# Performance work log

Measured on AMD Instinct MI355X. Metric: run time of the kernel, lower is better.

The kernel has to match this reference:

```python
import jax, jax.numpy as jnp
import numpy as np

D = 1024      # embed_dim
E = 2048      # expand * embed_dim
S_DIM = 128   # shrunken attn dim s
C = 256       # chunk size
SRC = 4096    # src_len
G = SRC // C  # num chunks
B = 8
STD = 0.02


def setup_inputs() -> dict:
    key = jax.random.key(0)
    ks = jax.random.split(key, 16)
    n = lambda k, shp: jax.random.normal(k, shp, dtype=jnp.float32)
    inp = {
        "query": n(ks[0], (SRC, B, D)),
        "key":   n(ks[1], (SRC, B, D)),
        "value": n(ks[2], (SRC, B, D)),
        # learned params (torch Linear stored as [in, out])
        "Wxs": n(ks[3], (D, S_DIM)) * STD, "bxs": n(ks[4], (S_DIM,)) * STD,
        "Wve": n(ks[5], (D, E)) * STD,     "bve": n(ks[6], (E,)) * STD,
        "Wue": n(ks[7], (D, E)) * STD,     "bue": n(ks[8], (E,)) * STD,
        "Wod": n(ks[9], (E, D)) * STD,     "bod": n(ks[10], (D,)) * STD,
        "rel_bias": n(ks[11], (C,)) * STD,
        "gamma": n(ks[12], (4, S_DIM)) * STD,
        "beta":  n(ks[13], (4, S_DIM)) * STD,
    }
    return inp


def reference(query, key, value, Wxs, bxs, Wve, bve, Wue, bue, Wod, bod,
              rel_bias, gamma, beta):
    # [S, B, D] -> [B, G, C, D]
    x = jnp.transpose(value, (1, 0, 2)).reshape(B, G, C, D)
    v = jnp.tanh(x @ Wve + bve)          # [b,g,c,e]
    z = jnp.tanh(x @ Wxs + bxs)          # [b,g,c,s]
    q_quad = z * gamma[0] + beta[0]
    k_quad = z * gamma[1] + beta[1]
    q_lin  = z * gamma[2] + beta[2]
    k_lin  = z * gamma[3] + beta[3]
    # local quadratic attention: relu(qk + bias)^2
    qk = jnp.einsum('bgns,bgms->bgnm', q_quad, k_quad)
    a = jnp.square(jax.nn.relu(qk + rel_bias))
    v_quad = jnp.einsum('bgnm,bgme->bgne', a, v)
    # global linear attention
    kv = jnp.einsum('bgcs,bgce->bse', k_lin, v)
    v_lin = jnp.einsum('bgcs,bse->bgce', q_lin, kv)
    u = jnp.tanh(x @ Wue + bue)          # [b,g,c,e]
    o = (u * (v_quad + v_lin)) @ Wod + bod   # [b,g,c,d]
    o = o.reshape(B, G * C, D)
    return jnp.transpose(o, (1, 0, 2))   # [S, B, D]
```

## Files before the change

### kernel.cpp

```cpp
#include <hip/hip_runtime.h>
#include <hip/hip_bf16.h>

using u16 = unsigned short;
using u32 = unsigned int;

typedef __attribute__((ext_vector_type(8))) short bf8;
typedef __attribute__((ext_vector_type(4))) float f4;
typedef __attribute__((ext_vector_type(4))) u16  us4;

#define DEV static __device__ __forceinline__

DEV float bf2f(u16 u) { return __uint_as_float(((u32)u) << 16); }
DEV u16 f2bf(float f) {
    u32 x = __float_as_uint(f);
    x += 0x7FFFu + ((x >> 16) & 1u);
    return (u16)(x >> 16);
}
DEV float tanhf_fast(float x) {
    float e = __expf(2.0f * x);
    return 1.0f - 2.0f / (e + 1.0f);
}
DEV f4 MFMA(bf8 a, bf8 b, f4 c) {
    return __builtin_amdgcn_mfma_f32_16x16x32_bf16(a, b, c, 0, 0, 0);
}
DEV int xcd_swz(int bx, int nwg) { return (bx & 7) * (nwg >> 3) + (bx >> 3); }

DEV void gload16(const u16* src, u16* dst) {
    __builtin_amdgcn_global_load_lds(
        (const __attribute__((address_space(1))) void*)src,
        (__attribute__((address_space(3))) void*)dst, 16, 0, 0);
}

#define SBAR()  __builtin_amdgcn_s_barrier()
#define SCHED() __builtin_amdgcn_sched_barrier(0)


#define WS_XB    ((size_t)0)
#define WS_WXST  ((size_t)67108864)
#define WS_WVET  ((size_t)67371008)
#define WS_WUET  ((size_t)71565312)
#define WS_WODT  ((size_t)75759616)
#define WS_KVT   ((size_t)79953920)
#define WS_A     ((size_t)84148224)
#define WS_QL    ((size_t)100925440)
#define WS_VT    ((size_t)109314048)
#define WS_T1    ((size_t)243531776)
#define WS_Z     ((size_t)243531776)
#define WS_KLT   ((size_t)251920384)
#define WS_QQ    ((size_t)260308992)
#define WS_KQ    ((size_t)268697600)
#define WS_KVF   ((size_t)277086208)

DEV void stage128x64(const u16* __restrict__ gbase, int ld, u16* lds, int w, int lane) {
    const int srow = lane >> 3;
    const int scol = ((lane & 7) ^ srow) * 8;
    #pragma unroll
    for (int i = 0; i < 4; i++) {
        const int rt = (i * 4 + w) * 8 + srow;
        gload16(gbase + (size_t)rt * ld + scol, lds + (size_t)(i * 4 + w) * 512);
    }
}

DEV void frag_mfma_64_swz(const u16* As, const u16* Bs, int wm, int wn, int ln, int lh,
                          f4 acc[4][4]) {
    #pragma unroll
    for (int kk2 = 0; kk2 < 2; kk2++) {
        const int sx = (((kk2 << 2) + lh) ^ (ln & 7)) << 3;
        bf8 a[4], b[4];
        #pragma unroll
        for (int mt = 0; mt < 4; mt++)
            a[mt] = *reinterpret_cast<const bf8*>(As + (wm * 64 + mt * 16 + ln) * 64 + sx);
        #pragma unroll
        for (int nt = 0; nt < 4; nt++)
            b[nt] = *reinterpret_cast<const bf8*>(Bs + (wn * 64 + nt * 16 + ln) * 64 + sx);
        #pragma unroll
        for (int mt = 0; mt < 4; mt++)
            #pragma unroll
            for (int nt = 0; nt < 4; nt++)
                acc[mt][nt] = MFMA(a[mt], b[nt], acc[mt][nt]);
    }
}

template<int NT, typename FA, typename FB>
DEV void gemm_pipe(FA stageA, FB stageB, u16* As, u16* Bs,
                   int wm, int wn, int ln, int lh, f4 acc[4][4]) {
    stageA(As, 0); stageB(Bs, 0);
    #pragma unroll 2
    for (int t = 0; t + 1 < NT; ++t) {
        u16* An = As + ((t & 1) ^ 1) * 8192;
        u16* Bn = Bs + ((t & 1) ^ 1) * 8192;
        stageA(An, t + 1); stageB(Bn, t + 1);
        asm volatile("s_waitcnt vmcnt(8)" ::: "memory");
        SBAR(); SCHED();
        frag_mfma_64_swz(As + (t & 1) * 8192, Bs + (t & 1) * 8192, wm, wn, ln, lh, acc);
        SCHED(); SBAR(); SCHED();
    }
    asm volatile("s_waitcnt vmcnt(0)" ::: "memory");
    SBAR();
    frag_mfma_64_swz(As + ((NT - 1) & 1) * 8192, Bs + ((NT - 1) & 1) * 8192, wm, wn, ln, lh, acc);
    SBAR();
}


#define T256 16384

DEV void stage2(const u16* __restrict__ gbase, int ld, u16* lds, int tid, int i0, int i1) {
    const int slot = tid & 7;
    {
        const int row = i0 * 64 + (tid >> 3);
        gload16(gbase + (size_t)row * ld + ((slot ^ (row & 7)) << 3),
                lds + ((size_t)(i0 * 512 + (tid & ~63)) << 3));
    }
    {
        const int row = i1 * 64 + (tid >> 3);
        gload16(gbase + (size_t)row * ld + ((slot ^ (row & 7)) << 3),
                lds + ((size_t)(i1 * 512 + (tid & ~63)) << 3));
    }
}

DEV const bf8* frag_ptr(const u16* base, int row, int ks, int lh) {
    const int slot = ((ks << 2) + lh) ^ (row & 7);
    return reinterpret_cast<const bf8*>(base + row * 64 + slot * 8);
}

template<int NT, typename FA, typename FB>
DEV void gemm_pipe8(FA sA, FB sB, u16* As, u16* Bs,
                    int wm, int wn, int ln, int lh, f4 acc[8][4]) {
    sA(As, 0, 0, 2); sA(As, 0, 1, 3); sB(Bs, 0, 0, 1); sB(Bs, 0, 2, 3);
    if (NT > 1) {
        sA(As + T256, 1, 0, 2); sA(As + T256, 1, 1, 3);
        sB(Bs + T256, 1, 0, 1); sB(Bs + T256, 1, 2, 3);
        asm volatile("s_waitcnt vmcnt(8)" ::: "memory");
    } else {
        asm volatile("s_waitcnt vmcnt(0)" ::: "memory");
    }
    SBAR(); SCHED();
    #pragma unroll 2
    for (int t = 0; t < NT; ++t) {
        const int c = t & 1;
        const u16* Ab = As + c * T256;
        const u16* Bb = Bs + c * T256;
        u16* Ac = As + c * T256;
        u16* Bc = Bs + c * T256;
        bf8 aR[8], b0[4], b1[4];
        #pragma unroll
        for (int j = 0; j < 4; j++) {
            aR[j]     = *frag_ptr(Ab, wm * 128 + j * 16 + ln, 0, lh);
            aR[4 + j] = *frag_ptr(Ab, wm * 128 + j * 16 + ln, 1, lh);
        }
        #pragma unroll
        for (int k = 0; k < 2; k++) {
            b0[k]     = *frag_ptr(Bb, wn * 64 + k * 16 + ln, 0, lh);
            b0[2 + k] = *frag_ptr(Bb, wn * 64 + k * 16 + ln, 1, lh);
        }
        SBAR(); SCHED();
        __builtin_amdgcn_s_setprio(1);
        #pragma unroll
        for (int j = 0; j < 4; j++) { acc[j][0] = MFMA(aR[j], b0[0], acc[j][0]);
                                      acc[j][1] = MFMA(aR[j], b0[1], acc[j][1]); }
        #pragma unroll
        for (int j = 0; j < 4; j++) { acc[j][0] = MFMA(aR[4 + j], b0[2], acc[j][0]);
                                      acc[j][1] = MFMA(aR[4 + j], b0[3], acc[j][1]); }
        __builtin_amdgcn_s_setprio(0);
        SCHED();
        #pragma unroll
        for (int k = 0; k < 2; k++) {
            b1[k]     = *frag_ptr(Bb, wn * 64 + (2 + k) * 16 + ln, 0, lh);
            b1[2 + k] = *frag_ptr(Bb, wn * 64 + (2 + k) * 16 + ln, 1, lh);
        }
        SBAR(); SCHED();
        __builtin_amdgcn_s_setprio(1);
        #pragma unroll
        for (int j = 0; j < 4; j++) { acc[j][2] = MFMA(aR[j], b1[0], acc[j][2]);
                                      acc[j][3] = MFMA(aR[j], b1[1], acc[j][3]); }
        #pragma unroll
        for (int j = 0; j < 4; j++) { acc[j][2] = MFMA(aR[4 + j], b1[2], acc[j][2]);
                                      acc[j][3] = MFMA(aR[4 + j], b1[3], acc[j][3]); }
        __builtin_amdgcn_s_setprio(0);
        SCHED();
        #pragma unroll
        for (int j = 0; j < 4; j++) {
            aR[j]     = *frag_ptr(Ab, wm * 128 + 64 + j * 16 + ln, 0, lh);
            aR[4 + j] = *frag_ptr(Ab, wm * 128 + 64 + j * 16 + ln, 1, lh);
        }
        if (t + 2 < NT) { sA(Ac, t + 2, 0, 2); sB(Bc, t + 2, 0, 1); }
        SBAR(); SCHED();
        __builtin_amdgcn_s_setprio(1);
        #pragma unroll
        for (int j = 0; j < 4; j++) { acc[4 + j][0] = MFMA(aR[j], b0[0], acc[4 + j][0]);
                                      acc[4 + j][1] = MFMA(aR[j], b0[1], acc[4 + j][1]); }
        #pragma unroll
        for (int j = 0; j < 4; j++) { acc[4 + j][0] = MFMA(aR[4 + j], b0[2], acc[4 + j][0]);
                                      acc[4 + j][1] = MFMA(aR[4 + j], b0[3], acc[4 + j][1]); }
        __builtin_amdgcn_s_setprio(0);
        SCHED();
        if (t + 2 < NT) {
            sA(Ac, t + 2, 1, 3); sB(Bc, t + 2, 2, 3);
            asm volatile("s_waitcnt vmcnt(8)" ::: "memory");
        } else if (t + 1 < NT) {
            asm volatile("s_waitcnt vmcnt(0)" ::: "memory");
        }
        SBAR(); SCHED();
        __builtin_amdgcn_s_setprio(1);
        #pragma unroll
        for (int j = 0; j < 4; j++) { acc[4 + j][2] = MFMA(aR[j], b1[0], acc[4 + j][2]);
                                      acc[4 + j][3] = MFMA(aR[j], b1[1], acc[4 + j][3]); }
        #pragma unroll
        for (int j = 0; j < 4; j++) { acc[4 + j][2] = MFMA(aR[4 + j], b1[2], acc[4 + j][2]);
                                      acc[4 + j][3] = MFMA(aR[4 + j], b1[3], acc[4 + j][3]); }
        __builtin_amdgcn_s_setprio(0);
        SCHED();
    }
}

__global__ void k_cvt_x(const float* __restrict__ src, u16* __restrict__ dst) {
    int m = blockIdx.x;
    int s = m >> 3, b = m & 7;
    const float* in = src + (size_t)m * 1024;
    u16* outp = dst + (((size_t)b << 12) + s) * 1024;
    int t = threadIdx.x * 4;
    float4 v = *reinterpret_cast<const float4*>(in + t);
    us4 o; o[0] = f2bf(v.x); o[1] = f2bf(v.y); o[2] = f2bf(v.z); o[3] = f2bf(v.w);
    *reinterpret_cast<us4*>(outp + t) = o;
}

__global__ void k_transpose(const float* __restrict__ src, u16* __restrict__ dst, int R, int C) {
    __shared__ u16 tile[32][33];
    int tx = threadIdx.x & 31, ty = threadIdx.x >> 5;
    int r0 = blockIdx.y * 32, c0 = blockIdx.x * 32;
    #pragma unroll
    for (int rr = ty; rr < 32; rr += 8)
        tile[rr][tx] = f2bf(src[(size_t)(r0 + rr) * C + c0 + tx]);
    __syncthreads();
    #pragma unroll
    for (int cc = ty; cc < 32; cc += 8)
        dst[(size_t)(c0 + cc) * R + r0 + tx] = tile[tx][cc];
}

__global__ void k_klinT(const u16* __restrict__ z, const float* __restrict__ gamma,
                        const float* __restrict__ beta, u16* __restrict__ klt) {
    __shared__ u16 tile[32][33];
    int tx = threadIdx.x & 31, ty = threadIdx.x >> 5;
    int r0 = blockIdx.x * 32;
    int c0 = blockIdx.y * 32;
    float gs = gamma[384 + c0 + tx], bs = beta[384 + c0 + tx];
    #pragma unroll
    for (int rr = ty; rr < 32; rr += 8) {
        u16 zv = z[(size_t)(r0 + rr) * 128 + c0 + tx];
        tile[rr][tx] = f2bf(bf2f(zv) * gs + bs);
    }
    __syncthreads();
    int b = r0 >> 12;
    int pos0 = r0 & 4095;
    #pragma unroll
    for (int cc = ty; cc < 32; cc += 8)
        klt[(((size_t)b * 128 + c0 + cc) << 12) + pos0 + tx] = tile[tx][cc];
}

__global__ __launch_bounds__(256) void k_zgemm(const u16* __restrict__ xb, const u16* __restrict__ WxsT,
                                               const float* __restrict__ bxs,
                                               const float* __restrict__ gamma, const float* __restrict__ beta,
                                               u16* __restrict__ z, u16* __restrict__ qq,
                                               u16* __restrict__ kq, u16* __restrict__ ql) {
    __shared__ u16 As[2][128 * 64];
    __shared__ u16 Bs[2][128 * 64];
    const int tid = threadIdx.x;
    const int lane = tid & 63, w = tid >> 6;
    const int ln = lane & 15, lh = lane >> 4;
    const int wm = w >> 1, wn = w & 1;
    const int rowbase = xcd_swz(blockIdx.x, 256) * 128;
    const u16* Ab = xb + (size_t)rowbase * 1024;
    f4 acc[4][4] = {};
    gemm_pipe<16>(
        [&](u16* l, int t) { stage128x64(Ab + t * 64, 1024, l, w, lane); },
        [&](u16* l, int t) { stage128x64(WxsT + t * 64, 1024, l, w, lane); },
        As[0], Bs[0], wm, wn, ln, lh, acc);
    #pragma unroll
    for (int mt = 0; mt < 4; mt++)
        #pragma unroll
        for (int nt = 0; nt < 4; nt++) {
            int col = wn * 64 + nt * 16 + ln;
            float bias = bxs[col];
            float g0 = gamma[col],       b0 = beta[col];
            float g1 = gamma[128 + col], b1 = beta[128 + col];
            float g2 = gamma[256 + col], b2 = beta[256 + col];
            int r0 = rowbase + wm * 64 + mt * 16 + lh * 4;
            #pragma unroll
            for (int rg = 0; rg < 4; rg++) {
                float zv = tanhf_fast(acc[mt][nt][rg] + bias);
                size_t idx = ((size_t)(r0 + rg) << 7) + col;
                z[idx]  = f2bf(zv);
                qq[idx] = f2bf(zv * g0 + b0);
                kq[idx] = f2bf(zv * g1 + b1);
                ql[idx] = f2bf(zv * g2 + b2);
            }
        }
}

__global__ __launch_bounds__(512, 2) void k_vgemm(const u16* __restrict__ xb, const u16* __restrict__ WveT,
                                                  const float* __restrict__ bve, u16* __restrict__ vT) {
    __shared__ u16 As[2 * T256];
    __shared__ u16 Bs[2 * T256];
    const int tid = threadIdx.x;
    const int lane = tid & 63, w = tid >> 6;
    const int ln = lane & 15, lh = lane >> 4;
    const int wm = w >> 2, wn = w & 3;
    const int rowbase = xcd_swz(blockIdx.x, 128) * 256;
    const int colbase = blockIdx.y * 256;
    const u16* Ag = xb + (size_t)rowbase * 1024;
    const u16* Bg = WveT + (size_t)colbase * 1024;
    f4 acc[8][4] = {};
    gemm_pipe8<16>(
        [&](u16* l, int t, int i0, int i1) { stage2(Ag + t * 64, 1024, l, tid, i0, i1); },
        [&](u16* l, int t, int i0, int i1) { stage2(Bg + t * 64, 1024, l, tid, i0, i1); },
        As, Bs, wm, wn, ln, lh, acc);
    #pragma unroll
    for (int mt = 0; mt < 8; mt++)
        #pragma unroll
        for (int nt = 0; nt < 4; nt++) {
            int e = colbase + wn * 64 + nt * 16 + ln;
            float bias = bve[e];
            int r0 = rowbase + wm * 128 + mt * 16 + lh * 4;
            int bb = r0 >> 12, s0 = r0 & 4095;
            us4 p;
            #pragma unroll
            for (int rg = 0; rg < 4; rg++) p[rg] = f2bf(tanhf_fast(acc[mt][nt][rg] + bias));
            *reinterpret_cast<us4*>(vT + (((size_t)bb * 2048 + e) << 12) + s0) = p;
        }
}

__global__ __launch_bounds__(256) void k_kv(const u16* __restrict__ vT, const u16* __restrict__ klt,
                                            float* __restrict__ kvF) {
    __shared__ u16 As[2][128 * 64];
    __shared__ u16 Bs[2][128 * 64];
    const int tid = threadIdx.x;
    const int lane = tid & 63, w = tid >> 6;
    const int ln = lane & 15, lh = lane >> 4;
    const int wm = w >> 1, wn = w & 1;
    const int b = blockIdx.z;
    const int rowbase = blockIdx.x * 128;
    const int kbase = blockIdx.y * 1024;
    const u16* Ab = vT + ((size_t)b * 2048 + rowbase) * 4096 + kbase;
    const u16* Bb = klt + ((size_t)b * 128) * 4096 + kbase;
    f4 acc[4][4] = {};
    gemm_pipe<16>(
        [&](u16* l, int t) { stage128x64(Ab + t * 64, 4096, l, w, lane); },
        [&](u16* l, int t) { stage128x64(Bb + t * 64, 4096, l, w, lane); },
        As[0], Bs[0], wm, wn, ln, lh, acc);
    #pragma unroll
    for (int mt = 0; mt < 4; mt++)
        #pragma unroll
        for (int nt = 0; nt < 4; nt++) {
            int s = wn * 64 + nt * 16 + ln;
            int e0 = rowbase + wm * 64 + mt * 16 + lh * 4;
            #pragma unroll
            for (int rg = 0; rg < 4; rg++)
                atomicAdd(&kvF[(((size_t)b * 2048 + e0 + rg) << 7) + s], acc[mt][nt][rg]);
        }
}

__global__ void k_kvcvt(const float* __restrict__ kvF, u16* __restrict__ kvT, int n) {
    int i = (blockIdx.x * blockDim.x + threadIdx.x) * 4;
    if (i < n) {
        float4 v = *reinterpret_cast<const float4*>(kvF + i);
        us4 o; o[0] = f2bf(v.x); o[1] = f2bf(v.y); o[2] = f2bf(v.z); o[3] = f2bf(v.w);
        *reinterpret_cast<us4*>(kvT + i) = o;
    }
}

__global__ __launch_bounds__(256) void k_a(const u16* __restrict__ qq, const u16* __restrict__ kq,
                                           const float* __restrict__ rel_bias, u16* __restrict__ a_out) {
    const int lane = threadIdx.x & 63, wid = threadIdx.x >> 6;
    const int ln = lane & 15, lh = lane >> 4;
    const int wm = wid >> 1, wn = wid & 1;
    const int ci = blockIdx.y;
    const int qbase = blockIdx.x * 128 + wm * 64;
    const int nbase = wn * 128;
    const int rowbase = ci << 8;
    f4 acc[4][8] = {};
    const u16* qr[4];
    #pragma unroll
    for (int mt = 0; mt < 4; mt++) qr[mt] = qq + ((size_t)(rowbase + qbase + mt * 16 + ln) << 7);
    const u16* kr[8];
    #pragma unroll
    for (int nt = 0; nt < 8; nt++) kr[nt] = kq + ((size_t)(rowbase + nbase + nt * 16 + ln) << 7);
    #pragma unroll
    for (int kk = 0; kk < 128; kk += 32) {
        int k0 = kk + lh * 8;
        bf8 aq[4], ak[8];
        #pragma unroll
        for (int mt = 0; mt < 4; mt++) aq[mt] = *reinterpret_cast<const bf8*>(qr[mt] + k0);
        #pragma unroll
        for (int nt = 0; nt < 8; nt++) ak[nt] = *reinterpret_cast<const bf8*>(kr[nt] + k0);
        #pragma unroll
        for (int mt = 0; mt < 4; mt++)
            #pragma unroll
            for (int nt = 0; nt < 8; nt++)
                acc[mt][nt] = MFMA(aq[mt], ak[nt], acc[mt][nt]);
    }
    #pragma unroll
    for (int nt = 0; nt < 8; nt++) {
        int key = nbase + nt * 16 + ln;
        float rb = rel_bias[key];
        #pragma unroll
        for (int mt = 0; mt < 4; mt++) {
            int r0 = qbase + mt * 16 + lh * 4;
            #pragma unroll
            for (int rg = 0; rg < 4; rg++) {
                float v = acc[mt][nt][rg] + rb;
                v = fmaxf(v, 0.0f); v = v * v;
                a_out[((size_t)ci << 16) + ((size_t)(r0 + rg) << 8) + key] = f2bf(v);
            }
        }
    }
}

__global__ __launch_bounds__(512, 2) void k_t1(const u16* __restrict__ ql, const u16* __restrict__ a_in,
                                               const u16* __restrict__ vT, const u16* __restrict__ kvT,
                                               u16* __restrict__ t1) {
    __shared__ u16 As[2 * T256];
    __shared__ u16 Bs[2 * T256];
    const int tid = threadIdx.x;
    const int lane = tid & 63, w = tid >> 6;
    const int ln = lane & 15, lh = lane >> 4;
    const int wm = w >> 2, wn = w & 3;
    const int ci = xcd_swz(blockIdx.x, 128);
    const int rowbase = ci << 8;
    const int ebase = blockIdx.y * 256;
    const int b = ci >> 4, g = ci & 15;
    const u16* Aa = ql + (size_t)rowbase * 128;
    const u16* Ba = kvT + ((size_t)(b * 2048 + ebase)) * 128;
    const u16* Ab2 = a_in + ((size_t)ci << 16);
    const u16* Bb2 = vT + ((size_t)(b * 2048 + ebase)) * 4096 + (g << 8);
    f4 acc[8][4] = {};
    gemm_pipe8<6>(
        [&](u16* l, int t, int i0, int i1) {
            if (t < 2) stage2(Aa + t * 64, 128, l, tid, i0, i1);
            else       stage2(Ab2 + (t - 2) * 64, 256, l, tid, i0, i1);
        },
        [&](u16* l, int t, int i0, int i1) {
            if (t < 2) stage2(Ba + t * 64, 128, l, tid, i0, i1);
            else       stage2(Bb2 + (t - 2) * 64, 4096, l, tid, i0, i1);
        },
        As, Bs, wm, wn, ln, lh, acc);
    #pragma unroll
    for (int mt = 0; mt < 8; mt++)
        #pragma unroll
        for (int nt = 0; nt < 4; nt++) {
            int e = ebase + wn * 64 + nt * 16 + ln;
            int r0 = rowbase + wm * 128 + mt * 16 + lh * 4;
            #pragma unroll
            for (int rg = 0; rg < 4; rg++)
                t1[((size_t)(r0 + rg) << 11) + e] = f2bf(acc[mt][nt][rg]);
        }
}

__global__ __launch_bounds__(512, 2) void k_u(const u16* __restrict__ xb, const u16* __restrict__ WueT,
                                              const float* __restrict__ bue, u16* t1) {
    __shared__ u16 As[2 * T256];
    __shared__ u16 Bs[2 * T256];
    const int tid = threadIdx.x;
    const int lane = tid & 63, w = tid >> 6;
    const int ln = lane & 15, lh = lane >> 4;
    const int wm = w >> 2, wn = w & 3;
    const int rowbase = xcd_swz(blockIdx.x, 128) * 256;
    const int colbase = blockIdx.y * 256;
    const u16* Ag = xb + (size_t)rowbase * 1024;
    const u16* Bg = WueT + (size_t)colbase * 1024;
    f4 acc[8][4] = {};
    gemm_pipe8<16>(
        [&](u16* l, int t, int i0, int i1) { stage2(Ag + t * 64, 1024, l, tid, i0, i1); },
        [&](u16* l, int t, int i0, int i1) { stage2(Bg + t * 64, 1024, l, tid, i0, i1); },
        As, Bs, wm, wn, ln, lh, acc);
    #pragma unroll
    for (int mt = 0; mt < 8; mt++)
        #pragma unroll
        for (int nt = 0; nt < 4; nt++) {
            int e = colbase + wn * 64 + nt * 16 + ln;
            float bias = bue[e];
            int r0 = rowbase + wm * 128 + mt * 16 + lh * 4;
            #pragma unroll
            for (int rg = 0; rg < 4; rg++) {
                size_t idx = ((size_t)(r0 + rg) << 11) + e;
                float t = bf2f(t1[idx]);
                float u = tanhf_fast(acc[mt][nt][rg] + bias);
                t1[idx] = f2bf(u * t);
            }
        }
}

__global__ __launch_bounds__(512, 2) void k_o(const u16* __restrict__ t1, const u16* __restrict__ WodT,
                                              const float* __restrict__ bod, float* __restrict__ out) {
    __shared__ u16 As[2 * T256];
    __shared__ u16 Bs[2 * T256];
    const int tid = threadIdx.x;
    const int lane = tid & 63, w = tid >> 6;
    const int ln = lane & 15, lh = lane >> 4;
    const int wm = w >> 2, wn = w & 3;
    const int rowbase = xcd_swz(blockIdx.x, 128) * 256;
    const int colbase = blockIdx.y * 256;
    const u16* Ag = t1 + (size_t)rowbase * 2048;
    const u16* Bg = WodT + (size_t)colbase * 2048;
    f4 acc[8][4] = {};
    gemm_pipe8<32>(
        [&](u16* l, int t, int i0, int i1) { stage2(Ag + t * 64, 2048, l, tid, i0, i1); },
        [&](u16* l, int t, int i0, int i1) { stage2(Bg + t * 64, 2048, l, tid, i0, i1); },
        As, Bs, wm, wn, ln, lh, acc);
    #pragma unroll
    for (int mt = 0; mt < 8; mt++)
        #pragma unroll
        for (int nt = 0; nt < 4; nt++) {
            int d = colbase + wn * 64 + nt * 16 + ln;
            float bias = bod[d];
            int r0 = rowbase + wm * 128 + mt * 16 + lh * 4;
            #pragma unroll
            for (int rg = 0; rg < 4; rg++) {
                int r = r0 + rg;
                int s = r & 4095, bb = r >> 12;
                out[((size_t)(s * 8 + bb) << 10) + d] = acc[mt][nt][rg] + bias;
            }
        }
}

extern "C" void kernel_launch(void* const* d_in, const int* in_sizes, int n_in,
                              void* d_out, int out_size, void* d_ws, size_t ws_size,
                              hipStream_t stream) {
    const float* value = (const float*)d_in[2];
    const float* Wxs = (const float*)d_in[3];  const float* bxs = (const float*)d_in[4];
    const float* Wve = (const float*)d_in[5];  const float* bve = (const float*)d_in[6];
    const float* Wue = (const float*)d_in[7];  const float* bue = (const float*)d_in[8];
    const float* Wod = (const float*)d_in[9];  const float* bod = (const float*)d_in[10];
    const float* rel_bias = (const float*)d_in[11];
    const float* gamma = (const float*)d_in[12];
    const float* beta  = (const float*)d_in[13];
    float* out = (float*)d_out;

    char* ws = (char*)d_ws;
    u16* xb   = (u16*)(ws + WS_XB);
    u16* WxsT = (u16*)(ws + WS_WXST);
    u16* WveT = (u16*)(ws + WS_WVET);
    u16* WueT = (u16*)(ws + WS_WUET);
    u16* WodT = (u16*)(ws + WS_WODT);
    u16* kvT  = (u16*)(ws + WS_KVT);
    u16* a    = (u16*)(ws + WS_A);
    u16* ql   = (u16*)(ws + WS_QL);
    u16* vT   = (u16*)(ws + WS_VT);
    u16* t1   = (u16*)(ws + WS_T1);
    u16* z    = (u16*)(ws + WS_Z);
    u16* klt  = (u16*)(ws + WS_KLT);
    u16* qq   = (u16*)(ws + WS_QQ);
    u16* kq   = (u16*)(ws + WS_KQ);
    float* kvF = (float*)(ws + WS_KVF);

    k_cvt_x<<<32768, 256, 0, stream>>>(value, xb);
    k_transpose<<<dim3(4, 32),  256, 0, stream>>>(Wxs, WxsT, 1024, 128);
    k_transpose<<<dim3(64, 32), 256, 0, stream>>>(Wve, WveT, 1024, 2048);
    k_transpose<<<dim3(64, 32), 256, 0, stream>>>(Wue, WueT, 1024, 2048);
    k_transpose<<<dim3(32, 64), 256, 0, stream>>>(Wod, WodT, 2048, 1024);
    k_zgemm<<<256, 256, 0, stream>>>(xb, WxsT, bxs, gamma, beta, z, qq, kq, ql);
    k_klinT<<<dim3(1024, 4), 256, 0, stream>>>(z, gamma, beta, klt);
    k_vgemm<<<dim3(128, 8), 512, 0, stream>>>(xb, WveT, bve, vT);
    hipMemsetAsync(kvF, 0, (size_t)8 * 2048 * 128 * 4, stream);
    k_kv<<<dim3(16, 4, 8), 256, 0, stream>>>(vT, klt, kvF);
    k_kvcvt<<<2048, 256, 0, stream>>>(kvF, kvT, 8 * 2048 * 128);
    k_a<<<dim3(2, 128), 256, 0, stream>>>(qq, kq, rel_bias, a);
    k_t1<<<dim3(128, 8), 512, 0, stream>>>(ql, a, vT, kvT, t1);
    k_u<<<dim3(128, 8), 512, 0, stream>>>(xb, WueT, bue, t1);
    k_o<<<dim3(128, 4), 512, 0, stream>>>(t1, WodT, bod, out);
}
```

Baseline: 750.6 us.

## Make big GEMMs persistent with 256 blocks looping over column tiles

The v, u and output projection GEMMs now launch 256 workgroups (one per CU on the device) instead of 1024 or 512. Each workgroup keeps its row tile and walks several 256-wide column tiles inside one continuous software pipeline. A per-tile epilogue writes results and resets the accumulators between tiles. The aim is to remove tail effects and the pipeline prologue and epilogue drains at tile boundaries, and to reuse the A rows from cache. The cost is that epilogue stores now sit inside the pipelined loop and may stall it, and the old XCD swizzle is replaced by a new block mapping.

```diff
diff --git a/kernel.cpp b/kernel.cpp
--- a/kernel.cpp
+++ b/kernel.cpp
@@ -24,6 +24,10 @@
     return __builtin_amdgcn_mfma_f32_16x16x32_bf16(a, b, c, 0, 0, 0);
 }
 DEV int xcd_swz(int bx, int nwg) { return (bx & 7) * (nwg >> 3) + (bx >> 3); }
+DEV void persist_map(int bx, int& row, int& grp) {
+    row = ((bx >> 3) << 2) | ((bx >> 1) & 3);
+    grp = bx & 1;
+}
 
 DEV void gload16(const u16* src, u16* dst) {
     __builtin_amdgcn_global_load_lds(
@@ -123,9 +127,10 @@
     return reinterpret_cast<const bf8*>(base + row * 64 + slot * 8);
 }
 
-template<int NT, typename FA, typename FB>
-DEV void gemm_pipe8(FA sA, FB sB, u16* As, u16* Bs,
+template<int NT, int PSHIFT, typename FA, typename FB, typename FE>
+DEV void gemm_pipe8(FA sA, FB sB, FE epi, u16* As, u16* Bs,
                     int wm, int wn, int ln, int lh, f4 acc[8][4]) {
+    constexpr int PMASK = (1 << PSHIFT) - 1;
     sA(As, 0, 0, 2); sA(As, 0, 1, 3); sB(Bs, 0, 0, 1); sB(Bs, 0, 2, 3);
     if (NT > 1) {
         sA(As + T256, 1, 0, 2); sA(As + T256, 1, 1, 3);
@@ -135,9 +140,7 @@
         asm volatile("s_waitcnt vmcnt(0)" ::: "memory");
     }
     SBAR(); SCHED();
-    #pragma unroll 2
-    for (int t = 0; t < NT; ++t) {
-        const int c = t & 1;
+    auto body = [&](int t, const int c) {
         const u16* Ab = As + c * T256;
         const u16* Bb = Bs + c * T256;
         u16* Ac = As + c * T256;
@@ -210,6 +213,12 @@
                                       acc[4 + j][3] = MFMA(aR[4 + j], b1[3], acc[4 + j][3]); }
         __builtin_amdgcn_s_setprio(0);
         SCHED();
+    };
+    for (int t = 0; t < NT; t += 2) {
+        body(t, 0);
+        if ((t & PMASK) == PMASK) epi(t >> PSHIFT);
+        body(t + 1, 1);
+        if (((t + 1) & PMASK) == PMASK) epi((t + 1) >> PSHIFT);
     }
 }
 
@@ -305,28 +314,37 @@
     const int lane = tid & 63, w = tid >> 6;
     const int ln = lane & 15, lh = lane >> 4;
     const int wm = w >> 2, wn = w & 3;
-    const int rowbase = xcd_swz(blockIdx.x, 128) * 256;
-    const int colbase = blockIdx.y * 256;
+    int rowt, grp;
+    persist_map(blockIdx.x, rowt, grp);
+    const int rowbase = rowt * 256;
+    const int grpcol = grp * 1024;
     const u16* Ag = xb + (size_t)rowbase * 1024;
-    const u16* Bg = WveT + (size_t)colbase * 1024;
+    const u16* Bg = WveT + (size_t)grpcol * 1024;
     f4 acc[8][4] = {};
-    gemm_pipe8<16>(
-        [&](u16* l, int t, int i0, int i1) { stage2(Ag + t * 64, 1024, l, tid, i0, i1); },
-        [&](u16* l, int t, int i0, int i1) { stage2(Bg + t * 64, 1024, l, tid, i0, i1); },
+    gemm_pipe8<64, 4>(
+        [&](u16* l, int T, int i0, int i1) { stage2(Ag + (T & 15) * 64, 1024, l, tid, i0, i1); },
+        [&](u16* l, int T, int i0, int i1) {
+            stage2(Bg + (((size_t)(T >> 4)) << 18) + (T & 15) * 64, 1024, l, tid, i0, i1); },
+        [&](int p) {
+            const int colbase = grpcol + p * 256;
+            #pragma unroll
+            for (int mt = 0; mt < 8; mt++)
+                #pragma unroll
+                for (int nt = 0; nt < 4; nt++) {
+                    int e = colbase + wn * 64 + nt * 16 + ln;
+                    float bias = bve[e];
+                    int r0 = rowbase + wm * 128 + mt * 16 + lh * 4;
+                    int bb = r0 >> 12, s0 = r0 & 4095;
+                    us4 pk;
+                    #pragma unroll
+                    for (int rg = 0; rg < 4; rg++) {
+                        pk[rg] = f2bf(tanhf_fast(acc[mt][nt][rg] + bias));
+                        acc[mt][nt][rg] = 0.0f;
+                    }
+                    *reinterpret_cast<us4*>(vT + (((size_t)bb * 2048 + e) << 12) + s0) = pk;
+                }
+        },
         As, Bs, wm, wn, ln, lh, acc);
-    #pragma unroll
-    for (int mt = 0; mt < 8; mt++)
-        #pragma unroll
-        for (int nt = 0; nt < 4; nt++) {
-            int e = colbase + wn * 64 + nt * 16 + ln;
-            float bias = bve[e];
-            int r0 = rowbase + wm * 128 + mt * 16 + lh * 4;
-            int bb = r0 >> 12, s0 = r0 & 4095;
-            us4 p;
-            #pragma unroll
-            for (int rg = 0; rg < 4; rg++) p[rg] = f2bf(tanhf_fast(acc[mt][nt][rg] + bias));
-            *reinterpret_cast<us4*>(vT + (((size_t)bb * 2048 + e) << 12) + s0) = p;
-        }
 }
 
 __global__ __launch_bounds__(256) void k_kv(const u16* __restrict__ vT, const u16* __restrict__ klt,
@@ -433,7 +451,7 @@
     const u16* Ab2 = a_in + ((size_t)ci << 16);
     const u16* Bb2 = vT + ((size_t)(b * 2048 + ebase)) * 4096 + (g << 8);
     f4 acc[8][4] = {};
-    gemm_pipe8<6>(
+    gemm_pipe8<6, 10>(
         [&](u16* l, int t, int i0, int i1) {
             if (t < 2) stage2(Aa + t * 64, 128, l, tid, i0, i1);
             else       stage2(Ab2 + (t - 2) * 64, 256, l, tid, i0, i1);
@@ -442,6 +460,7 @@
             if (t < 2) stage2(Ba + t * 64, 128, l, tid, i0, i1);
             else       stage2(Bb2 + (t - 2) * 64, 4096, l, tid, i0, i1);
         },
+        [&](int) {},
         As, Bs, wm, wn, ln, lh, acc);
     #pragma unroll
     for (int mt = 0; mt < 8; mt++)
@@ -463,30 +482,37 @@
     const int lane = tid & 63, w = tid >> 6;
     const int ln = lane & 15, lh = lane >> 4;
     const int wm = w >> 2, wn = w & 3;
-    const int rowbase = xcd_swz(blockIdx.x, 128) * 256;
-    const int colbase = blockIdx.y * 256;
+    int rowt, grp;
+    persist_map(blockIdx.x, rowt, grp);
+    const int rowbase = rowt * 256;
+    const int grpcol = grp * 1024;
     const u16* Ag = xb + (size_t)rowbase * 1024;
-    const u16* Bg = WueT + (size_t)colbase * 1024;
+    const u16* Bg = WueT + (size_t)grpcol * 1024;
     f4 acc[8][4] = {};
-    gemm_pipe8<16>(
-        [&](u16* l, int t, int i0, int i1) { stage2(Ag + t * 64, 1024, l, tid, i0, i1); },
-        [&](u16* l, int t, int i0, int i1) { stage2(Bg + t * 64, 1024, l, tid, i0, i1); },
+    gemm_pipe8<64, 4>(
+        [&](u16* l, int T, int i0, int i1) { stage2(Ag + (T & 15) * 64, 1024, l, tid, i0, i1); },
+        [&](u16* l, int T, int i0, int i1) {
+            stage2(Bg + (((size_t)(T >> 4)) << 18) + (T & 15) * 64, 1024, l, tid, i0, i1); },
+        [&](int p) {
+            const int colbase = grpcol + p * 256;
+            #pragma unroll
+            for (int mt = 0; mt < 8; mt++)
+                #pragma unroll
+                for (int nt = 0; nt < 4; nt++) {
+                    int e = colbase + wn * 64 + nt * 16 + ln;
+                    float bias = bue[e];
+                    int r0 = rowbase + wm * 128 + mt * 16 + lh * 4;
+                    #pragma unroll
+                    for (int rg = 0; rg < 4; rg++) {
+                        size_t idx = ((size_t)(r0 + rg) << 11) + e;
+                        float t = bf2f(t1[idx]);
+                        float u = tanhf_fast(acc[mt][nt][rg] + bias);
+                        t1[idx] = f2bf(u * t);
+                        acc[mt][nt][rg] = 0.0f;
+                    }
+                }
+        },
         As, Bs, wm, wn, ln, lh, acc);
-    #pragma unroll
-    for (int mt = 0; mt < 8; mt++)
-        #pragma unroll
-        for (int nt = 0; nt < 4; nt++) {
-            int e = colbase + wn * 64 + nt * 16 + ln;
-            float bias = bue[e];
-            int r0 = rowbase + wm * 128 + mt * 16 + lh * 4;
-            #pragma unroll
-            for (int rg = 0; rg < 4; rg++) {
-                size_t idx = ((size_t)(r0 + rg) << 11) + e;
-                float t = bf2f(t1[idx]);
-                float u = tanhf_fast(acc[mt][nt][rg] + bias);
-                t1[idx] = f2bf(u * t);
-            }
-        }
 }
 
 __global__ __launch_bounds__(512, 2) void k_o(const u16* __restrict__ t1, const u16* __restrict__ WodT,
@@ -497,29 +523,36 @@
     const int lane = tid & 63, w = tid >> 6;
     const int ln = lane & 15, lh = lane >> 4;
     const int wm = w >> 2, wn = w & 3;
-    const int rowbase = xcd_swz(blockIdx.x, 128) * 256;
-    const int colbase = blockIdx.y * 256;
+    int rowt, grp;
+    persist_map(blockIdx.x, rowt, grp);
+    const int rowbase = rowt * 256;
+    const int grpcol = grp * 512;
     const u16* Ag = t1 + (size_t)rowbase * 2048;
-    const u16* Bg = WodT + (size_t)colbase * 2048;
+    const u16* Bg = WodT + (size_t)grpcol * 2048;
     f4 acc[8][4] = {};
-    gemm_pipe8<32>(
-        [&](u16* l, int t, int i0, int i1) { stage2(Ag + t * 64, 2048, l, tid, i0, i1); },
-        [&](u16* l, int t, int i0, int i1) { stage2(Bg + t * 64, 2048, l, tid, i0, i1); },
+    gemm_pipe8<64, 5>(
+        [&](u16* l, int T, int i0, int i1) { stage2(Ag + (T & 31) * 64, 2048, l, tid, i0, i1); },
+        [&](u16* l, int T, int i0, int i1) {
+            stage2(Bg + (size_t)(T >> 5) * 524288 + (T & 31) * 64, 2048, l, tid, i0, i1); },
+        [&](int p) {
+            const int colbase = grpcol + p * 256;
+            #pragma unroll
+            for (int mt = 0; mt < 8; mt++)
+                #pragma unroll
+                for (int nt = 0; nt < 4; nt++) {
+                    int d = colbase + wn * 64 + nt * 16 + ln;
+                    float bias = bod[d];
+                    int r0 = rowbase + wm * 128 + mt * 16 + lh * 4;
+                    #pragma unroll
+                    for (int rg = 0; rg < 4; rg++) {
+                        int r = r0 + rg;
+                        int s = r & 4095, bb = r >> 12;
+                        out[((size_t)(s * 8 + bb) << 10) + d] = acc[mt][nt][rg] + bias;
+                        acc[mt][nt][rg] = 0.0f;
+                    }
+                }
+        },
         As, Bs, wm, wn, ln, lh, acc);
-    #pragma unroll
-    for (int mt = 0; mt < 8; mt++)
-        #pragma unroll
-        for (int nt = 0; nt < 4; nt++) {
-            int d = colbase + wn * 64 + nt * 16 + ln;
-            float bias = bod[d];
-            int r0 = rowbase + wm * 128 + mt * 16 + lh * 4;
-            #pragma unroll
-            for (int rg = 0; rg < 4; rg++) {
-                int r = r0 + rg;
-                int s = r & 4095, bb = r >> 12;
-                out[((size_t)(s * 8 + bb) << 10) + d] = acc[mt][nt][rg] + bias;
-            }
-        }
 }
 
 extern "C" void kernel_launch(void* const* d_in, const int* in_sizes, int n_in,
@@ -559,12 +592,12 @@
     k_transpose<<<dim3(32, 64), 256, 0, stream>>>(Wod, WodT, 2048, 1024);
     k_zgemm<<<256, 256, 0, stream>>>(xb, WxsT, bxs, gamma, beta, z, qq, kq, ql);
     k_klinT<<<dim3(1024, 4), 256, 0, stream>>>(z, gamma, beta, klt);
-    k_vgemm<<<dim3(128, 8), 512, 0, stream>>>(xb, WveT, bve, vT);
+    k_vgemm<<<256, 512, 0, stream>>>(xb, WveT, bve, vT);
     hipMemsetAsync(kvF, 0, (size_t)8 * 2048 * 128 * 4, stream);
     k_kv<<<dim3(16, 4, 8), 256, 0, stream>>>(vT, klt, kvF);
     k_kvcvt<<<2048, 256, 0, stream>>>(kvF, kvT, 8 * 2048 * 128);
     k_a<<<dim3(2, 128), 256, 0, stream>>>(qq, kq, rel_bias, a);
     k_t1<<<dim3(128, 8), 512, 0, stream>>>(ql, a, vT, kvT, t1);
-    k_u<<<dim3(128, 8), 512, 0, stream>>>(xb, WueT, bue, t1);
-    k_o<<<dim3(128, 4), 512, 0, stream>>>(t1, WodT, bod, out);
-}
+    k_u<<<256, 512, 0, stream>>>(xb, WueT, bue, t1);
+    k_o<<<256, 512, 0, stream>>>(t1, WodT, bod, out);
+}
```

After: 878.6 us. 17.1% more time.
